# Kernel optimization log

Measured on AMD Instinct MI355X. Metric: run time of the kernel, lower is better.

Reference implementation:

```python
import jax, jax.numpy as jnp
import numpy as np

T, B, V, D, H, L = 256, 32, 32000, 256, 256, 2  # seq, batch, vocab, embed, hidden, layers
INIT_U = 0.1


def setup_inputs() -> dict:
    key = jax.random.key(0)
    k0, k1, k2, k3, k4 = jax.random.split(key, 5)
    input_ids = jax.random.randint(k0, (T, B), 0, V)
    emb = jax.random.uniform(k1, (V, D), minval=-INIT_U, maxval=INIT_U, dtype=jnp.float32)
    Wi = jax.random.uniform(k2, (L, H, H), minval=-INIT_U, maxval=INIT_U, dtype=jnp.float32)  # dim==hidden
    Wh = jax.random.uniform(k3, (L, H, H), minval=-INIT_U, maxval=INIT_U, dtype=jnp.float32)
    bh = jnp.zeros((L, H), jnp.float32)
    decW = jax.random.uniform(k4, (V, H), minval=-INIT_U, maxval=INIT_U, dtype=jnp.float32)
    decB = jnp.zeros((V,), jnp.float32)
    return {"input_ids": input_ids, "emb": emb, "Wi": Wi, "Wh": Wh, "bh": bh, "decW": decW, "decB": decB}


def reference(input_ids, emb, Wi, Wh, bh, decW, decB):
    # Embedding lookup (dropout is identity in eval mode)
    e_seq = emb[input_ids]                      # [T, B, D]
    h0 = jnp.zeros((L, B, H), e_seq.dtype)      # hidden init per layer

    def step(hidden, e_t):
        e = e_t
        new_h = []
        for l in range(L):  # small fixed layer loop
            h = jax.nn.sigmoid(e @ Wi[l] + hidden[l] @ Wh[l] + bh[l])
            new_h.append(h)
            e = h
        return jnp.stack(new_h), e

    hidden, out = jax.lax.scan(step, h0, e_seq)  # out: [T, B, H]
    decoded = out @ decW.T + decB                # [T, B, V]
    return decoded, hidden
```

## Files before the change

kernel.cpp:

```cpp
#include <hip/hip_runtime.h>

typedef unsigned short u16;
typedef unsigned int   u32;
typedef unsigned long long u64;
typedef __attribute__((ext_vector_type(2)))  u32  u32x2;
typedef __attribute__((ext_vector_type(4)))  float f32x4;
typedef __attribute__((ext_vector_type(16))) float f32x16;
typedef __attribute__((ext_vector_type(8)))  short b16x8;

#define T_ 256
#define B_ 32
#define V_ 32000
#define H_ 256

__device__ __forceinline__ u16 f2bf(float f){
  union { float fv; u32 uv; } v; v.fv = f;
  return (u16)((v.uv + 0x7FFFu + ((v.uv >> 16) & 1u)) >> 16);
}
__device__ __forceinline__ float bf2f(short x){
  union { float fv; u32 uv; } c; c.uv = ((u32)(u16)x) << 16; return c.fv;
}
__device__ __forceinline__ float sigm_fast(float z){
  return __builtin_amdgcn_rcpf(1.0f + __builtin_amdgcn_exp2f(z * -1.44269504f));
}
__device__ __forceinline__ b16x8 ald16(const u16* p){
  union { u64 q[2]; b16x8 v; } u;
  const u64* q = (const u64*)p;
  u.q[0] = __hip_atomic_load(q,     __ATOMIC_RELAXED, __HIP_MEMORY_SCOPE_AGENT);
  u.q[1] = __hip_atomic_load(q + 1, __ATOMIC_RELAXED, __HIP_MEMORY_SCOPE_AGENT);
  return u.v;
}
__device__ __forceinline__ void ast16(u16* p, b16x8 v){
  union { u64 q[2]; b16x8 v; } u; u.v = v;
  u64* q = (u64*)p;
  __hip_atomic_store(q,     u.q[0], __ATOMIC_RELAXED, __HIP_MEMORY_SCOPE_AGENT);
  __hip_atomic_store(q + 1, u.q[1], __ATOMIC_RELAXED, __HIP_MEMORY_SCOPE_AGENT);
}

__global__ __launch_bounds__(256)
void prep_kernel(const float* __restrict__ Wi, const float* __restrict__ Wh,
                 const float* __restrict__ decW,
                 u16* __restrict__ decWb, u16* __restrict__ wt,
                 u32* __restrict__ flags){
  if (blockIdx.x == 0 && threadIdx.x == 0){ flags[0] = 0; flags[1] = 0; }
  const int NDECG = (V_ * H_) / 8;
  const int NWTG  = (4 * H_ * H_) / 8;
  const int g = blockIdx.x * blockDim.x + threadIdx.x;
  if (g < NDECG){
    const float* s = decW + (size_t)g * 8;
    f32x4 a = *(const f32x4*)(s);
    f32x4 b = *(const f32x4*)(s + 4);
    union { u16 h[8]; b16x8 v; } o;
    #pragma unroll
    for (int u = 0; u < 4; ++u){
      o.h[u]     = f2bf(a[u]);
      o.h[4 + u] = f2bf(b[u]);
    }
    *(b16x8*)(decWb + (size_t)g * 8) = o.v;
  } else if (g < NDECG + NWTG){
    const int j0 = (g - NDECG) * 8;
    const int m  = j0 >> 16;
    const int r  = j0 & 65535;
    const int row = r >> 8;
    const int k0  = r & 255;
    const float* src = (m == 0) ? Wh
                     : (m == 1) ? (Wi + H_ * H_)
                     : (m == 2) ? (Wh + H_ * H_)
                     :            Wi;
    union { u16 h[8]; b16x8 v; } o;
    #pragma unroll
    for (int u = 0; u < 8; ++u)
      o.h[u] = f2bf(src[(k0 + u) * H_ + row]);
    *(b16x8*)(wt + j0) = o.v;
  }
}


__global__ __launch_bounds__(256, 2)
void x0_kernel(const int* __restrict__ ids, const float* __restrict__ emb,
               const u16* __restrict__ WiT0, const float* __restrict__ bh,
               float* __restrict__ xp){
  const int tid = threadIdx.x, w = tid >> 6, l = tid & 63;
  const int lr = l & 15, lh = l >> 4;
  const int t = blockIdx.x;

  b16x8 wA[4][8];
  #pragma unroll
  for (int nt = 0; nt < 4; ++nt){
    const int col = w * 64 + nt * 16 + lr;
    #pragma unroll
    for (int ks = 0; ks < 8; ++ks)
      wA[nt][ks] = *(const b16x8*)(WiT0 + (size_t)col * H_ + ks * 32 + lh * 8);
  }

  const int b0 = ids[t * B_ + lr];
  const int b1 = ids[t * B_ + 16 + lr];
  const float* er0 = emb + (size_t)b0 * H_;
  const float* er1 = emb + (size_t)b1 * H_;

  f32x4 acc[2][4];
  #pragma unroll
  for (int nt = 0; nt < 4; ++nt){
    f32x4 bs = *(const f32x4*)(bh + w * 64 + nt * 16 + lh * 4);
    acc[0][nt] = bs;
    acc[1][nt] = bs;
  }

  #pragma unroll
  for (int ks = 0; ks < 8; ++ks){
    b16x8 e[2];
    {
      f32x4 a0 = *(const f32x4*)(er0 + ks * 32 + lh * 8);
      f32x4 a1 = *(const f32x4*)(er0 + ks * 32 + lh * 8 + 4);
      f32x4 c0 = *(const f32x4*)(er1 + ks * 32 + lh * 8);
      f32x4 c1 = *(const f32x4*)(er1 + ks * 32 + lh * 8 + 4);
      #pragma unroll
      for (int i2 = 0; i2 < 4; ++i2){
        e[0][i2] = (short)f2bf(a0[i2]); e[0][4 + i2] = (short)f2bf(a1[i2]);
        e[1][i2] = (short)f2bf(c0[i2]); e[1][4 + i2] = (short)f2bf(c1[i2]);
      }
    }
    #pragma unroll
    for (int nt = 0; nt < 4; ++nt){
      acc[0][nt] = __builtin_amdgcn_mfma_f32_16x16x32_bf16(wA[nt][ks], e[0], acc[0][nt], 0, 0, 0);
      acc[1][nt] = __builtin_amdgcn_mfma_f32_16x16x32_bf16(wA[nt][ks], e[1], acc[1][nt], 0, 0, 0);
    }
  }
  #pragma unroll
  for (int mt = 0; mt < 2; ++mt)
    #pragma unroll
    for (int nt = 0; nt < 4; ++nt)
      *(f32x4*)(xp + (size_t)t * 8192 + mt * 4096 + w * 1024 + nt * 256 + lh * 64 + lr * 4)
          = acc[mt][nt];
}

__global__ __launch_bounds__(512, 1)
void mega_kernel(const u16* __restrict__ wt, const float* __restrict__ xp,
                 const float* __restrict__ bh,
                 u16* __restrict__ outseq, float* __restrict__ hid,
                 const u16* __restrict__ decWb, const float* __restrict__ decB,
                 float* __restrict__ out, u32* __restrict__ flags){
  __shared__ u16 smu[65536];
  char* smem = (char*)smu;
  const int tid = threadIdx.x, w = tid >> 6, l = tid & 63;
  const int bid = blockIdx.x;

  if (bid < 2){
    const int lr = l & 15, lh = l >> 4;

    const u16* whT0 = wt;
    const u16* wiT1 = wt + 65536;
    const u16* whT1 = wt + 131072;

    b16x8 wH0[2][8], wI1[2][8], wH1[2][8];
    #pragma unroll
    for (int nt = 0; nt < 2; ++nt){
      const int col = w * 32 + nt * 16 + lr;
      #pragma unroll
      for (int ks = 0; ks < 8; ++ks){
        wH0[nt][ks] = *(const b16x8*)(whT0 + (size_t)col * H_ + ks * 32 + lh * 8);
        wI1[nt][ks] = *(const b16x8*)(wiT1 + (size_t)col * H_ + ks * 32 + lh * 8);
        wH1[nt][ks] = *(const b16x8*)(whT1 + (size_t)col * H_ + ks * 32 + lh * 8);
      }
    }
    f32x4 bs1[2];
    #pragma unroll
    for (int nt = 0; nt < 2; ++nt)
      bs1[nt] = *(const f32x4*)(bh + H_ + w * 32 + nt * 16 + lh * 4);

    int ra[8];
    #pragma unroll
    for (int ks = 0; ks < 8; ++ks)
      ra[ks] = lr * 512 + ((ks * 64 + lh * 16) ^ ((lr & 7) << 4));

    int wrh[2];
    #pragma unroll
    for (int nt = 0; nt < 2; ++nt)
      wrh[nt] = lr * 512 + ((w * 64 + nt * 32 + lh * 8) ^ ((lr & 7) << 4));

    const int srow = tid >> 5, scolb = (tid & 31) * 16;
    const int sa = srow * 512 + (scolb ^ ((srow & 7) << 4));
    const size_t sgbase = (size_t)(bid * 16 + srow) * H_ + (tid & 31) * 8;

    const int xoff = bid * 4096 + w * 512 + lh * 64 + lr * 4;

    { u32* z = (u32*)smem;
      for (int i = tid; i < 8192; i += 512) z[i] = 0; }

    f32x4 xc0, xc1, xn0, xn1;
    xc0 = *(const f32x4*)(xp + xoff);
    xc1 = *(const f32x4*)(xp + xoff + 256);
    __syncthreads();

#define PACKW(DST, ADDR, V0, V1, V2, V3)                                        \
  { u32x2 pk;                                                                   \
    pk[0] = (u32)f2bf(V0) | ((u32)f2bf(V1) << 16);                              \
    pk[1] = (u32)f2bf(V2) | ((u32)f2bf(V3) << 16);                              \
    *(u32x2*)((DST) + (ADDR)) = pk; }

#define STEP(PAR, S)                                                            \
  {                                                                             \
    const char* rb0 = smem + (PAR) * 8192;                                      \
    const char* rb1 = smem + 16384 + (1 - (PAR)) * 8192;                        \
    if ((S) >= 2){                                                              \
      b16x8 v = *(const b16x8*)(rb1 + sa);                                      \
      ast16(outseq + (size_t)((S) - 2) * 8192 + sgbase, v);                     \
    }                                                                           \
    f32x4 c0 = (f32x4){}, c1 = (f32x4){};                                       \
    f32x4 d0 = bs1[0], d1 = bs1[1];                                             \
    _Pragma("unroll")                                                           \
    for (int ks = 0; ks < 8; ++ks){                                             \
      b16x8 a = *(const b16x8*)(rb0 + ra[ks]);                                  \
      c0 = __builtin_amdgcn_mfma_f32_16x16x32_bf16(wH0[0][ks], a, c0, 0, 0, 0); \
      c1 = __builtin_amdgcn_mfma_f32_16x16x32_bf16(wH0[1][ks], a, c1, 0, 0, 0); \
      d0 = __builtin_amdgcn_mfma_f32_16x16x32_bf16(wI1[0][ks], a, d0, 0, 0, 0); \
      d1 = __builtin_amdgcn_mfma_f32_16x16x32_bf16(wI1[1][ks], a, d1, 0, 0, 0); \
    }                                                                           \
    { const float* pn = xp + (size_t)(((S) < 255) ? (S) + 1 : 255) * 8192 + xoff; \
      xn0 = *(const f32x4*)(pn);                                                \
      xn1 = *(const f32x4*)(pn + 256); }                                        \
    { char* wb0 = smem + (1 - (PAR)) * 8192;                                    \
      PACKW(wb0, wrh[0], sigm_fast(c0[0] + xc0[0]), sigm_fast(c0[1] + xc0[1]),  \
                         sigm_fast(c0[2] + xc0[2]), sigm_fast(c0[3] + xc0[3]))  \
      PACKW(wb0, wrh[1], sigm_fast(c1[0] + xc1[0]), sigm_fast(c1[1] + xc1[1]),  \
                         sigm_fast(c1[2] + xc1[2]), sigm_fast(c1[3] + xc1[3]))  \
    }                                                                           \
    if ((S) >= 1){                                                              \
      _Pragma("unroll")                                                         \
      for (int ks = 0; ks < 8; ++ks){                                           \
        b16x8 a = *(const b16x8*)(rb1 + ra[ks]);                                \
        d0 = __builtin_amdgcn_mfma_f32_16x16x32_bf16(wH1[0][ks], a, d0, 0, 0, 0); \
        d1 = __builtin_amdgcn_mfma_f32_16x16x32_bf16(wH1[1][ks], a, d1, 0, 0, 0); \
      }                                                                         \
      char* wb1 = smem + 16384 + (PAR) * 8192;                                  \
      PACKW(wb1, wrh[0], sigm_fast(d0[0]), sigm_fast(d0[1]),                    \
                         sigm_fast(d0[2]), sigm_fast(d0[3]))                    \
      PACKW(wb1, wrh[1], sigm_fast(d1[0]), sigm_fast(d1[1]),                    \
                         sigm_fast(d1[2]), sigm_fast(d1[3]))                    \
    }                                                                           \
    xc0 = xn0; xc1 = xn1;                                                       \
    __syncthreads();                                                            \
  }

    for (int s2 = 0; s2 < 128; ++s2){
      const int s = s2 * 2;
      STEP(0, s)
      STEP(1, s + 1)
      if (tid == 0)
        __hip_atomic_store(&flags[bid], (u32)(s2 * 2), __ATOMIC_RELAXED,
                           __HIP_MEMORY_SCOPE_AGENT);
    }
#undef STEP

    {
      const char* rb0 = smem;
      const char* rb1 = smem + 16384 + 8192;
      { b16x8 v = *(const b16x8*)(rb1 + sa);
        ast16(outseq + (size_t)254 * 8192 + sgbase, v); }

      f32x4 d0 = bs1[0], d1 = bs1[1];
      #pragma unroll
      for (int ks = 0; ks < 8; ++ks){
        b16x8 a0 = *(const b16x8*)(rb0 + ra[ks]);
        b16x8 a1 = *(const b16x8*)(rb1 + ra[ks]);
        d0 = __builtin_amdgcn_mfma_f32_16x16x32_bf16(wI1[0][ks], a0, d0, 0, 0, 0);
        d1 = __builtin_amdgcn_mfma_f32_16x16x32_bf16(wI1[1][ks], a0, d1, 0, 0, 0);
        d0 = __builtin_amdgcn_mfma_f32_16x16x32_bf16(wH1[0][ks], a1, d0, 0, 0, 0);
        d1 = __builtin_amdgcn_mfma_f32_16x16x32_bf16(wH1[1][ks], a1, d1, 0, 0, 0);
      }
      { char* wb1 = smem + 16384;
        PACKW(wb1, wrh[0], sigm_fast(d0[0]), sigm_fast(d0[1]),
                           sigm_fast(d0[2]), sigm_fast(d0[3]))
        PACKW(wb1, wrh[1], sigm_fast(d1[0]), sigm_fast(d1[1]),
                           sigm_fast(d1[2]), sigm_fast(d1[3]))
      }
      __syncthreads();

      b16x8 h1v = *(const b16x8*)(smem + 16384 + sa);
      b16x8 h0v = *(const b16x8*)(smem + sa);
      ast16(outseq + (size_t)255 * 8192 + sgbase, h1v);
      float* hd0 = hid + sgbase;
      float* hd1 = hid + 8192 + sgbase;
      #pragma unroll
      for (int j = 0; j < 8; ++j){
        hd0[j] = bf2f(h0v[j]);
        hd1[j] = bf2f(h1v[j]);
      }
      __syncthreads();
      if (tid == 0)
        __hip_atomic_store(&flags[bid], 256u, __ATOMIC_RELAXED,
                           __HIP_MEMORY_SCOPE_AGENT);
    }
#undef PACKW
  } else {
    const int la = l & 31, hi = l >> 5;
    const int wm = w >> 2, wn = w & 3;

    const int idx = bid - 2;
    const int mb  = idx / 125;
    const int nb  = idx - mb * 125;

    if (tid == 0){
      const u32 need = (u32)(mb * 8 + 8);
      const u64* fl = (const u64*)flags;
      for (;;){
        u64 ff = __hip_atomic_load(fl, __ATOMIC_RELAXED, __HIP_MEMORY_SCOPE_AGENT);
        u32 f0 = (u32)ff, f1 = (u32)(ff >> 32);
        u32 got = f0 < f1 ? f0 : f1;
        if (got >= need) break;
        if (need - got > 24) __builtin_amdgcn_s_sleep(64);
        else                 __builtin_amdgcn_s_sleep(8);
      }
    }
    __syncthreads();

    const int srow = tid >> 3;
    const int sc   = tid & 7;
    const int scx  = sc ^ (srow & 7);
    const size_t gA = ((size_t)(mb * 256 + srow)) * H_ + sc * 8;
    const size_t gB = ((size_t)(nb * 256 + srow)) * H_ + sc * 8;
    const int    sl = srow * 128 + scx * 16;

    b16x8 rA[4], rB[4];
#define GLOADS(KK)                                                              \
  { _Pragma("unroll")                                                           \
    for (int s5 = 0; s5 < 4; ++s5){                                             \
      rA[s5] = ald16(outseq + gA + (size_t)s5 * 64 * H_ + (KK) * 64);           \
      rB[s5] = *(const b16x8*)(decWb + gB + (size_t)s5 * 64 * H_ + (KK) * 64);  \
    } }
#define DSWRITE(BUF)                                                            \
  { _Pragma("unroll")                                                           \
    for (int s5 = 0; s5 < 4; ++s5){                                             \
      *(b16x8*)(smem + (BUF) * 32768 + s5 * 8192 + sl)         = rA[s5];        \
      *(b16x8*)(smem + 65536 + (BUF) * 32768 + s5 * 8192 + sl) = rB[s5];        \
    } }

    const int aRow = wm * 128 + la;
    const int bRow = wn * 64 + la;
    int fOff[4];
    #pragma unroll
    for (int ks = 0; ks < 4; ++ks)
      fOff[ks] = ((ks * 32 + hi * 16) ^ ((la & 7) << 4));

    f32x16 acc[4][2];
    #pragma unroll
    for (int mt = 0; mt < 4; ++mt)
      #pragma unroll
      for (int nt = 0; nt < 2; ++nt)
        acc[mt][nt] = (f32x16){};

    GLOADS(0);
    #pragma unroll
    for (int kk = 0; kk < 4; ++kk){
      DSWRITE(kk & 1);
      if (kk < 3) GLOADS(kk + 1);
      __syncthreads();
      const char* bufA = smem + (kk & 1) * 32768;
      const char* bufB = smem + 65536 + (kk & 1) * 32768;
      #pragma unroll
      for (int ks = 0; ks < 4; ++ks){
        b16x8 aF[4], bF[2];
        #pragma unroll
        for (int mt = 0; mt < 4; ++mt)
          aF[mt] = *(const b16x8*)(bufA + (aRow + mt * 32) * 128 + fOff[ks]);
        #pragma unroll
        for (int nt = 0; nt < 2; ++nt)
          bF[nt] = *(const b16x8*)(bufB + (bRow + nt * 32) * 128 + fOff[ks]);
        #pragma unroll
        for (int mt = 0; mt < 4; ++mt)
          #pragma unroll
          for (int nt = 0; nt < 2; ++nt)
            acc[mt][nt] = __builtin_amdgcn_mfma_f32_32x32x16_bf16(aF[mt], bF[nt], acc[mt][nt], 0, 0, 0);
      }
      __syncthreads();
    }
#undef GLOADS
#undef DSWRITE

    #pragma unroll
    for (int nt = 0; nt < 2; ++nt){
      const int colg = nb * 256 + wn * 64 + nt * 32 + la;
      const float bias = decB[colg];
      #pragma unroll
      for (int mt = 0; mt < 4; ++mt){
        const int rowb = mb * 256 + wm * 128 + mt * 32 + hi * 4;
        #pragma unroll
        for (int r = 0; r < 16; ++r){
          const int rowg = rowb + (r & 3) + 8 * (r >> 2);
          __builtin_nontemporal_store(acc[mt][nt][r] + bias,
                                      &out[(size_t)rowg * V_ + colg]);
        }
      }
    }
  }
}

extern "C" void kernel_launch(void* const* d_in, const int* in_sizes, int n_in,
                              void* d_out, int out_size, void* d_ws, size_t ws_size,
                              hipStream_t stream){
  const int*   ids  = (const int*)  d_in[0];
  const float* emb  = (const float*)d_in[1];
  const float* Wi   = (const float*)d_in[2];
  const float* Wh   = (const float*)d_in[3];
  const float* bh   = (const float*)d_in[4];
  const float* decW = (const float*)d_in[5];
  const float* decB = (const float*)d_in[6];
  float* out = (float*)d_out;

  char* ws = (char*)d_ws;
  u16*  decWb  = (u16*)(ws);
  u16*  wt     = (u16*)(ws + 16384000);
  u16*  outseq = (u16*)(ws + 16908288);
  float* xp    = (float*)(ws + 21102592);
  u32*  flags  = (u32*)(ws + 29491200);

  float* hid = out + (size_t)T_ * B_ * V_;

  prep_kernel<<<4128, 256, 0, stream>>>(Wi, Wh, decW, decWb, wt, flags);
  x0_kernel<<<256, 256, 0, stream>>>(ids, emb, wt + 3 * H_ * H_, bh, xp);
  mega_kernel<<<4002, 512, 0, stream>>>(wt, xp, bh, outseq, hid,
                                        decWb, decB, out, flags);
}
```

Before: 415.6 us.

## Make decoder GEMM blocks persistent over N tiles with resident A rows

Decoder blocks now each own a 128-row slice of the hidden sequence, load it once into shared memory, and loop over several 256-column vocabulary tiles. B tiles are double-buffered, and the next tile's first chunk is prefetched across the tile boundary. The grid shrinks from 4002 to 1026 blocks, and each block waits for only 4 timesteps' worth of recurrence per slice, so decoding can begin earlier. This cuts repeated A reloads and block scheduling overhead, but each block holds a smaller 128x256 output tile, which raises the ratio of B loads to compute.

```diff
diff --git a/kernel.cpp b/kernel.cpp
--- a/kernel.cpp
+++ b/kernel.cpp
@@ -253,16 +253,14 @@
 #undef STEP
 
     {
-      const char* rb0 = smem;
-      const char* rb1 = smem + 16384 + 8192;
-      { b16x8 v = *(const b16x8*)(rb1 + sa);
+      { b16x8 v = *(const b16x8*)(smem + 16384 + 8192 + sa);
         ast16(outseq + (size_t)254 * 8192 + sgbase, v); }
 
       f32x4 d0 = bs1[0], d1 = bs1[1];
       #pragma unroll
       for (int ks = 0; ks < 8; ++ks){
-        b16x8 a0 = *(const b16x8*)(rb0 + ra[ks]);
-        b16x8 a1 = *(const b16x8*)(rb1 + ra[ks]);
+        b16x8 a0 = *(const b16x8*)(smem + ra[ks]);
+        b16x8 a1 = *(const b16x8*)(smem + 16384 + 8192 + ra[ks]);
         d0 = __builtin_amdgcn_mfma_f32_16x16x32_bf16(wI1[0][ks], a0, d0, 0, 0, 0);
         d1 = __builtin_amdgcn_mfma_f32_16x16x32_bf16(wI1[1][ks], a0, d1, 0, 0, 0);
         d0 = __builtin_amdgcn_mfma_f32_16x16x32_bf16(wH1[0][ks], a1, d0, 0, 0, 0);
@@ -296,12 +294,12 @@
     const int la = l & 31, hi = l >> 5;
     const int wm = w >> 2, wn = w & 3;
 
-    const int idx = bid - 2;
-    const int mb  = idx / 125;
-    const int nb  = idx - mb * 125;
+    const int idx  = bid - 2;
+    const int mb2  = idx >> 4;
+    const int slot = idx & 15;
 
     if (tid == 0){
-      const u32 need = (u32)(mb * 8 + 8);
+      const u32 need = (u32)(mb2 * 4 + 4);
       const u64* fl = (const u64*)flags;
       for (;;){
         u64 ff = __hip_atomic_load(fl, __ATOMIC_RELAXED, __HIP_MEMORY_SCOPE_AGENT);
@@ -314,84 +312,99 @@
     }
     __syncthreads();
 
-    const int srow = tid >> 3;
-    const int sc   = tid & 7;
-    const int scx  = sc ^ (srow & 7);
-    const size_t gA = ((size_t)(mb * 256 + srow)) * H_ + sc * 8;
-    const size_t gB = ((size_t)(nb * 256 + srow)) * H_ + sc * 8;
-    const int    sl = srow * 128 + scx * 16;
-
-    b16x8 rA[4], rB[4];
-#define GLOADS(KK)                                                              \
-  { _Pragma("unroll")                                                           \
-    for (int s5 = 0; s5 < 4; ++s5){                                             \
-      rA[s5] = ald16(outseq + gA + (size_t)s5 * 64 * H_ + (KK) * 64);           \
+    {
+      const int cA  = tid & 31;
+      const int rA0 = tid >> 5;
+      #pragma unroll
+      for (int j = 0; j < 8; ++j){
+        const int row = rA0 + 16 * j;
+        b16x8 v = ald16(outseq + (size_t)(mb2 * 128 + row) * H_ + cA * 8);
+        *(b16x8*)(smem + row * 512 + ((cA ^ (row & 7)) << 4)) = v;
+      }
+    }
+
+    const int srowB = tid >> 3;
+    const int scB   = tid & 7;
+    const int scxB  = scB ^ (srowB & 7);
+    const int slB   = srowB * 128 + scxB * 16;
+    b16x8 rB[4];
+#define BLOADS(NB, KK)                                                          \
+  do { const size_t gB = ((size_t)((NB) * 256 + srowB)) * H_ + scB * 8;         \
+    _Pragma("unroll")                                                           \
+    for (int s5 = 0; s5 < 4; ++s5)                                              \
       rB[s5] = *(const b16x8*)(decWb + gB + (size_t)s5 * 64 * H_ + (KK) * 64);  \
-    } }
-#define DSWRITE(BUF)                                                            \
-  { _Pragma("unroll")                                                           \
-    for (int s5 = 0; s5 < 4; ++s5){                                             \
-      *(b16x8*)(smem + (BUF) * 32768 + s5 * 8192 + sl)         = rA[s5];        \
-      *(b16x8*)(smem + 65536 + (BUF) * 32768 + s5 * 8192 + sl) = rB[s5];        \
-    } }
-
-    const int aRow = wm * 128 + la;
+  } while (0)
+#define BSWRITE(BUF)                                                            \
+  do { _Pragma("unroll")                                                        \
+    for (int s5 = 0; s5 < 4; ++s5)                                              \
+      *(b16x8*)(smem + 65536 + (BUF) * 32768 + s5 * 8192 + slB) = rB[s5];       \
+  } while (0)
+
+    const int aRow = wm * 64 + la;
     const int bRow = wn * 64 + la;
-    int fOff[4];
+    int fOffB[4];
     #pragma unroll
     for (int ks = 0; ks < 4; ++ks)
-      fOff[ks] = ((ks * 32 + hi * 16) ^ ((la & 7) << 4));
-
-    f32x16 acc[4][2];
-    #pragma unroll
-    for (int mt = 0; mt < 4; ++mt)
-      #pragma unroll
-      for (int nt = 0; nt < 2; ++nt)
-        acc[mt][nt] = (f32x16){};
-
-    GLOADS(0);
-    #pragma unroll
-    for (int kk = 0; kk < 4; ++kk){
-      DSWRITE(kk & 1);
-      if (kk < 3) GLOADS(kk + 1);
-      __syncthreads();
-      const char* bufA = smem + (kk & 1) * 32768;
-      const char* bufB = smem + 65536 + (kk & 1) * 32768;
-      #pragma unroll
-      for (int ks = 0; ks < 4; ++ks){
-        b16x8 aF[4], bF[2];
-        #pragma unroll
-        for (int mt = 0; mt < 4; ++mt)
-          aF[mt] = *(const b16x8*)(bufA + (aRow + mt * 32) * 128 + fOff[ks]);
+      fOffB[ks] = ((ks * 32 + hi * 16) ^ ((la & 7) << 4));
+
+    BLOADS(slot, 0);
+    for (int nb = slot; nb < 125; nb += 16){
+      f32x16 acc[2][2];
+      #pragma unroll
+      for (int mt = 0; mt < 2; ++mt)
         #pragma unroll
         for (int nt = 0; nt < 2; ++nt)
-          bF[nt] = *(const b16x8*)(bufB + (bRow + nt * 32) * 128 + fOff[ks]);
+          acc[mt][nt] = (f32x16){};
+
+      #pragma unroll
+      for (int kk = 0; kk < 4; ++kk){
+        BSWRITE(kk & 1);
+        if (kk < 3){
+          BLOADS(nb, kk + 1);
+        } else if (nb + 16 < 125){
+          BLOADS(nb + 16, 0);
+        }
+        __syncthreads();
+        const char* bufB = smem + 65536 + (kk & 1) * 32768;
         #pragma unroll
-        for (int mt = 0; mt < 4; ++mt)
+        for (int ks = 0; ks < 4; ++ks){
+          b16x8 aF[2], bF[2];
+          #pragma unroll
+          for (int mt = 0; mt < 2; ++mt){
+            const int row = aRow + mt * 32;
+            const int c   = kk * 8 + ks * 2 + hi;
+            aF[mt] = *(const b16x8*)(smem + row * 512 + ((c ^ (row & 7)) << 4));
+          }
           #pragma unroll
           for (int nt = 0; nt < 2; ++nt)
-            acc[mt][nt] = __builtin_amdgcn_mfma_f32_32x32x16_bf16(aF[mt], bF[nt], acc[mt][nt], 0, 0, 0);
-      }
-      __syncthreads();
-    }
-#undef GLOADS
-#undef DSWRITE
-
-    #pragma unroll
-    for (int nt = 0; nt < 2; ++nt){
-      const int colg = nb * 256 + wn * 64 + nt * 32 + la;
-      const float bias = decB[colg];
-      #pragma unroll
-      for (int mt = 0; mt < 4; ++mt){
-        const int rowb = mb * 256 + wm * 128 + mt * 32 + hi * 4;
+            bF[nt] = *(const b16x8*)(bufB + (bRow + nt * 32) * 128 + fOffB[ks]);
+          #pragma unroll
+          for (int mt = 0; mt < 2; ++mt)
+            #pragma unroll
+            for (int nt = 0; nt < 2; ++nt)
+              acc[mt][nt] = __builtin_amdgcn_mfma_f32_32x32x16_bf16(aF[mt], bF[nt], acc[mt][nt], 0, 0, 0);
+        }
+        __syncthreads();
+      }
+
+      #pragma unroll
+      for (int nt = 0; nt < 2; ++nt){
+        const int colg = nb * 256 + wn * 64 + nt * 32 + la;
+        const float bias = decB[colg];
         #pragma unroll
-        for (int r = 0; r < 16; ++r){
-          const int rowg = rowb + (r & 3) + 8 * (r >> 2);
-          __builtin_nontemporal_store(acc[mt][nt][r] + bias,
-                                      &out[(size_t)rowg * V_ + colg]);
+        for (int mt = 0; mt < 2; ++mt){
+          const int rowb = mb2 * 128 + wm * 64 + mt * 32 + hi * 4;
+          #pragma unroll
+          for (int r = 0; r < 16; ++r){
+            const int rowg = rowb + (r & 3) + 8 * (r >> 2);
+            __builtin_nontemporal_store(acc[mt][nt][r] + bias,
+                                        &out[(size_t)rowg * V_ + colg]);
+          }
         }
       }
     }
+#undef BLOADS
+#undef BSWRITE
   }
 }
 
@@ -418,6 +431,6 @@
 
   prep_kernel<<<4128, 256, 0, stream>>>(Wi, Wh, decW, decWb, wt, flags);
   x0_kernel<<<256, 256, 0, stream>>>(ids, emb, wt + 3 * H_ * H_, bh, xp);
-  mega_kernel<<<4002, 512, 0, stream>>>(wt, xp, bh, outseq, hid,
+  mega_kernel<<<1026, 512, 0, stream>>>(wt, xp, bh, outseq, hid,
                                         decWb, decB, out, flags);
 }
```

New measurement: 420.3 us. About the same (+1.1%).
